# Optimization experiments

Measured on AMD Instinct MI355X. Metric: run time of the kernel, lower is better.

The kernel has to match this reference:

```python
import jax, jax.numpy as jnp
import numpy as np

B, S, H = 2, 2048, 2048
E, I, TOPK = 8, 1408, 2


def setup_inputs() -> dict:
    key = jax.random.key(0)
    k0, k1, k2, k3, k4 = jax.random.split(key, 5)
    return {
        "hidden_states": jax.random.normal(k0, (B, S, H), dtype=jnp.float32),
        "Wr": jax.random.normal(k1, (H, E), dtype=jnp.float32) * 0.02,
        "Wg": jax.random.normal(k2, (E, H, I), dtype=jnp.float32) * 0.02,
        "Wu": jax.random.normal(k3, (E, H, I), dtype=jnp.float32) * 0.02,
        "Wd": jax.random.normal(k4, (E, I, H), dtype=jnp.float32) * 0.02,
    }


def reference(hidden_states, Wr, Wg, Wu, Wd):
    b, s, h = hidden_states.shape
    x = hidden_states.reshape(-1, h)                      # [T, H]
    T = x.shape[0]
    router_logits = x @ Wr                                # [T, E]
    probs = jax.nn.softmax(router_logits.astype(jnp.float32), axis=-1)
    top_w, top_i = jax.lax.top_k(probs, TOPK)             # [T, k]
    top_w = top_w / jnp.sum(top_w, axis=-1, keepdims=True)  # norm_topk_prob
    top_w = top_w.astype(x.dtype)
    # combine weights per (token, expert): zero where expert not selected
    cw = jnp.zeros((T, E), dtype=x.dtype).at[
        jnp.arange(T)[:, None], top_i].add(top_w)         # [T, E]
    # per-expert SwiGLU MLP computed densely, masked/weighted by cw
    g = jax.nn.silu(jnp.einsum('th,ehi->tei', x, Wg))     # [T, E, I]
    u = jnp.einsum('th,ehi->tei', x, Wu)                  # [T, E, I]
    y = jnp.einsum('tei,eih->teh', g * u, Wd)             # [T, E, H]
    out = jnp.einsum('te,teh->th', cw, y)                 # [T, H]
    return out.reshape(b, s, h), router_logits
```

## Files before the change

### kernel.cpp

```cpp
#include <hip/hip_runtime.h>

#define T_TOK 4096
#define HD 2048
#define NE 8
#define NI 1408

typedef __bf16 bf16x8 __attribute__((ext_vector_type(8)));
typedef float f32x4 __attribute__((ext_vector_type(4)));
typedef unsigned short ushort8 __attribute__((ext_vector_type(8)));

#define S_WAITCNT_VMCNT(n) asm volatile("s_waitcnt vmcnt(" #n ")" ::: "memory")
__device__ __forceinline__ void wave_barrier() {
  asm volatile("" ::: "memory");
  __builtin_amdgcn_s_barrier();
  asm volatile("" ::: "memory");
}

__device__ __forceinline__ unsigned short f2bf(float f) {
  unsigned int u = __float_as_uint(f);
  u += 0x7FFFu + ((u >> 16) & 1u);
  return (unsigned short)(u >> 16);
}
__device__ __forceinline__ float bf2f(unsigned short u) {
  return __uint_as_float((unsigned int)u << 16);
}

__device__ __forceinline__ void gload_lds16(const void* g, void* l) {
  __builtin_amdgcn_global_load_lds(
      (const __attribute__((address_space(1))) unsigned int*)g,
      (__attribute__((address_space(3))) unsigned int*)l, 16, 0, 0);
}

__device__ __forceinline__ void transpose_body(const float* s,
                                               unsigned short* d,
                                               int R, int C, int r0, int c0) {
  int tid = threadIdx.x;
  int rg = tid & 7, cg = tid >> 3;
  const float* sb = s + (size_t)(r0 + rg * 8) * C + c0 + cg * 4;
  f32x4 v[8];
#pragma unroll
  for (int j = 0; j < 8; j++) v[j] = *(const f32x4*)(sb + (size_t)j * C);
  unsigned short* db = d + (size_t)(c0 + cg * 4) * R + r0 + rg * 8;
#pragma unroll
  for (int cc = 0; cc < 4; cc++) {
    ushort8 o;
#pragma unroll
    for (int j = 0; j < 8; j++) o[j] = f2bf(v[j][cc]);
    *(ushort8*)(db + (size_t)cc * R) = o;
  }
}

__global__ void prepass_kernel(const float* __restrict__ x,
                               const float* __restrict__ Wr,
                               const float* __restrict__ Wg,
                               const float* __restrict__ Wu,
                               const float* __restrict__ Wd,
                               float* __restrict__ logits,
                               unsigned short* __restrict__ xbf,
                               unsigned short* __restrict__ Wgt,
                               unsigned short* __restrict__ Wut,
                               unsigned short* __restrict__ Wdt,
                               int4* __restrict__ tokinfo,
                               int* __restrict__ cnt) {
  const int bid = blockIdx.x;
  if (bid < 1024) {
    int wv = threadIdx.x >> 6, lane = threadIdx.x & 63;
    int t = bid * 4 + wv;
    const float* xr = x + (size_t)t * HD;
    unsigned short* xbr = xbf + (size_t)t * HD;
    float acc[NE];
#pragma unroll
    for (int e = 0; e < NE; e++) acc[e] = 0.f;
    for (int hi = 0; hi < HD / 256; hi++) {
      int h = hi * 256 + lane * 4;
      f32x4 xv = *(const f32x4*)(xr + h);
      ushort4 o = { f2bf(xv[0]), f2bf(xv[1]), f2bf(xv[2]), f2bf(xv[3]) };
      *(ushort4*)(xbr + h) = o;
#pragma unroll
      for (int j = 0; j < 4; j++) {
        const float4* w4 = (const float4*)(Wr + (size_t)(h + j) * NE);
        float4 a = w4[0], b = w4[1];
        float xs = xv[j];
        acc[0] += xs * a.x; acc[1] += xs * a.y; acc[2] += xs * a.z; acc[3] += xs * a.w;
        acc[4] += xs * b.x; acc[5] += xs * b.y; acc[6] += xs * b.z; acc[7] += xs * b.w;
      }
    }
#pragma unroll
    for (int m = 32; m > 0; m >>= 1) {
#pragma unroll
      for (int e = 0; e < NE; e++) acc[e] += __shfl_xor(acc[e], m, 64);
    }
    if (lane < NE) logits[(size_t)t * NE + lane] = acc[lane];
    if (lane == 0) {
      int e0 = 0;
#pragma unroll
      for (int e = 1; e < NE; e++) if (acc[e] > acc[e0]) e0 = e;
      int e1 = (e0 == 0) ? 1 : 0;
#pragma unroll
      for (int e = 0; e < NE; e++) if (e != e0 && acc[e] > acc[e1]) e1 = e;
      float ex = expf(acc[e1] - acc[e0]);
      float w0 = 1.f / (1.f + ex);
      float w1 = ex / (1.f + ex);
      atomicAdd(&cnt[e0], 1);
      atomicAdd(&cnt[e1], 1);
      tokinfo[t] = make_int4(e0, e1, __float_as_int(w0), __float_as_int(w1));
    }
  } else if (bid < 1024 + 5632) {
    int r = bid - 1024;
    int xt = r % 11; r /= 11;
    int yt = r % 32; r /= 32;
    int e = r >> 1, sel = r & 1;
    const float* sp = (sel ? Wu : Wg) + (size_t)e * HD * NI;
    unsigned short* dp = (sel ? Wut : Wgt) + (size_t)e * HD * NI;
    transpose_body(sp, dp, HD, NI, yt * 64, xt * 128);
  } else {
    int r = bid - 1024 - 5632;
    int xt = r % 16; r /= 16;
    int yt = r % 22; r /= 22;
    int e = r;
    const float* sp = Wd + (size_t)e * NI * HD;
    unsigned short* dp = Wdt + (size_t)e * NI * HD;
    transpose_body(sp, dp, NI, HD, yt * 64, xt * 128);
  }
}

__global__ void route_finalize_kernel(const int4* __restrict__ tokinfo,
                                      int* __restrict__ cnt,
                                      int* __restrict__ row_tok,
                                      int2* __restrict__ tok2row) {
  if (threadIdx.x == 0) {
    int o = 0;
    for (int e = 0; e < NE; e++) { cnt[8 + e] = o; o += cnt[e]; }
  }
  __syncthreads();
  for (int t = threadIdx.x; t < T_TOK; t += 1024) {
    int4 info = tokinfo[t];
    int p0 = atomicAdd(&cnt[16 + info.x], 1);
    int r0 = cnt[8 + info.x] + p0;
    row_tok[r0] = t;
    int p1 = atomicAdd(&cnt[16 + info.y], 1);
    int r1 = cnt[8 + info.y] + p1;
    row_tok[r1] = t;
    tok2row[t] = make_int2(r0, r1);
  }
}

__launch_bounds__(256, 2)
__global__ void gemm1_kernel(const unsigned short* __restrict__ xbf,
                             const unsigned short* __restrict__ Wgt,
                             const unsigned short* __restrict__ Wut,
                             unsigned short* __restrict__ act,
                             const int* __restrict__ row_tok,
                             const int* __restrict__ cnt) {
  const int f = blockIdx.x + 11 * (blockIdx.y + 32 * blockIdx.z);
  const int e = f & 7;
  const int rem = f >> 3;
  const int nt = rem >> 5;
  const int mt = rem & 31;
  const int c = cnt[e];
  if (mt * 128 >= c) return;
  const int off = cnt[8 + e];
  const int rowbase = off + mt * 128, rowend = off + c;
  const int i0 = nt * 128;
  __shared__ __align__(16) char smem[73728];
  const int lane = threadIdx.x & 63, w = threadIdx.x >> 6;
  const int wr = w >> 1, wc = w & 1;

  const int rr0 = w * 16 + (lane >> 2);
  const int rr1 = rr0 + 64;
  const int q0 = (lane & 3) ^ ((rr0 >> 1) & 3);
  const int q1 = (lane & 3) ^ ((rr1 >> 1) & 3);
  int g0 = rowbase + rr0; if (g0 > rowend - 1) g0 = rowend - 1;
  int g1 = rowbase + rr1; if (g1 > rowend - 1) g1 = rowend - 1;
  const size_t tokA0 = (size_t)row_tok[g0] * HD;
  const size_t tokA1 = (size_t)row_tok[g1] * HD;
  const size_t bB0 = ((size_t)e * NI + i0 + rr0) * HD;
  const size_t bB1 = ((size_t)e * NI + i0 + rr1) * HD;
  const int ldsA = w * 1024;

  f32x4 zero = {0.f, 0.f, 0.f, 0.f};
  f32x4 accg[4][4], accu[4][4];
#pragma unroll
  for (int a = 0; a < 4; a++)
#pragma unroll
    for (int b = 0; b < 4; b++) { accg[a][b] = zero; accu[a][b] = zero; }

  auto stage = [&](int buf, int ks) {
    const int k0 = ks * 32;
    char* base = smem + buf * 24576;
    gload_lds16(xbf + tokA0 + k0 + q0 * 8, base + ldsA);
    gload_lds16(xbf + tokA1 + k0 + q1 * 8, base + ldsA + 4096);
    gload_lds16(Wgt + bB0 + k0 + q0 * 8, base + 8192 + ldsA);
    gload_lds16(Wgt + bB1 + k0 + q1 * 8, base + 8192 + ldsA + 4096);
    gload_lds16(Wut + bB0 + k0 + q0 * 8, base + 16384 + ldsA);
    gload_lds16(Wut + bB1 + k0 + q1 * 8, base + 16384 + ldsA + 4096);
  };
  const int rl = lane & 15, kslot = lane >> 4;
  auto compute = [&](int buf) {
    const char* base = smem + buf * 24576;
    bf16x8 af[4], bg[4], bu[4];
#pragma unroll
    for (int mi = 0; mi < 4; mi++) {
      int r = wr * 64 + mi * 16 + rl;
      int byt = r * 64 + ((kslot ^ ((r >> 1) & 3)) << 4);
      af[mi] = *(const bf16x8*)(base + byt);
    }
#pragma unroll
    for (int ni = 0; ni < 4; ni++) {
      int r = wc * 64 + ni * 16 + rl;
      int byt = r * 64 + ((kslot ^ ((r >> 1) & 3)) << 4);
      bg[ni] = *(const bf16x8*)(base + 8192 + byt);
      bu[ni] = *(const bf16x8*)(base + 16384 + byt);
    }
#pragma unroll
    for (int mi = 0; mi < 4; mi++)
#pragma unroll
      for (int ni = 0; ni < 4; ni++) {
        accg[mi][ni] = __builtin_amdgcn_mfma_f32_16x16x32_bf16(af[mi], bg[ni], accg[mi][ni], 0, 0, 0);
        accu[mi][ni] = __builtin_amdgcn_mfma_f32_16x16x32_bf16(af[mi], bu[ni], accu[mi][ni], 0, 0, 0);
      }
  };

  stage(0, 0);
  stage(1, 1);
  const int NKS = HD / 32;
  for (int ks = 0; ks < NKS; ks++) {
    if (ks < NKS - 1) {
      S_WAITCNT_VMCNT(6);
    } else {
      S_WAITCNT_VMCNT(0);
    }
    wave_barrier();
    if (ks + 2 < NKS) stage((ks + 2) % 3, ks + 2);
    compute(ks % 3);
  }

  const int rh = lane >> 4;
#pragma unroll
  for (int mi = 0; mi < 4; mi++)
#pragma unroll
    for (int ni = 0; ni < 4; ni++)
#pragma unroll
      for (int j = 0; j < 4; j++) {
        int grow = rowbase + wr * 64 + mi * 16 + rh * 4 + j;
        if (grow < rowend) {
          int gcol = i0 + wc * 64 + ni * 16 + rl;
          float g = accg[mi][ni][j], u = accu[mi][ni][j];
          float val = g / (1.f + __expf(-g)) * u;
          act[(size_t)grow * NI + gcol] = f2bf(val);
        }
      }
}

__launch_bounds__(256, 3)
__global__ void gemm2_kernel(const unsigned short* __restrict__ act,
                             const unsigned short* __restrict__ Wdt,
                             unsigned short* __restrict__ y,
                             const int* __restrict__ cnt) {
  const int f = blockIdx.x + 16 * (blockIdx.y + 32 * blockIdx.z);
  const int e = f & 7;
  const int rem = f >> 3;
  const int nt = rem >> 5;
  const int mt = rem & 31;
  const int c = cnt[e];
  if (mt * 128 >= c) return;
  const int off = cnt[8 + e];
  const int rowbase = off + mt * 128, rowend = off + c;
  const int n0 = nt * 128;
  __shared__ __align__(16) char smem[49152];
  const int lane = threadIdx.x & 63, w = threadIdx.x >> 6;
  const int wr = w >> 1, wc = w & 1;

  const int rr0 = w * 16 + (lane >> 2);
  const int rr1 = rr0 + 64;
  const int q0 = (lane & 3) ^ ((rr0 >> 1) & 3);
  const int q1 = (lane & 3) ^ ((rr1 >> 1) & 3);
  int g0 = rowbase + rr0; if (g0 > rowend - 1) g0 = rowend - 1;
  int g1 = rowbase + rr1; if (g1 > rowend - 1) g1 = rowend - 1;
  const size_t aA0 = (size_t)g0 * NI;
  const size_t aA1 = (size_t)g1 * NI;
  const size_t bB0 = ((size_t)e * HD + n0 + rr0) * NI;
  const size_t bB1 = ((size_t)e * HD + n0 + rr1) * NI;
  const int ldsA = w * 1024;

  f32x4 zero = {0.f, 0.f, 0.f, 0.f};
  f32x4 acc[4][4];
#pragma unroll
  for (int a = 0; a < 4; a++)
#pragma unroll
    for (int b = 0; b < 4; b++) acc[a][b] = zero;

  auto stage = [&](int buf, int ks) {
    const int k0 = ks * 32;
    char* base = smem + buf * 16384;
    gload_lds16(act + aA0 + k0 + q0 * 8, base + ldsA);
    gload_lds16(act + aA1 + k0 + q1 * 8, base + ldsA + 4096);
    gload_lds16(Wdt + bB0 + k0 + q0 * 8, base + 8192 + ldsA);
    gload_lds16(Wdt + bB1 + k0 + q1 * 8, base + 8192 + ldsA + 4096);
  };
  const int rl = lane & 15, kslot = lane >> 4;
  auto compute = [&](int buf) {
    const char* base = smem + buf * 16384;
    bf16x8 af[4], bf[4];
#pragma unroll
    for (int mi = 0; mi < 4; mi++) {
      int r = wr * 64 + mi * 16 + rl;
      int byt = r * 64 + ((kslot ^ ((r >> 1) & 3)) << 4);
      af[mi] = *(const bf16x8*)(base + byt);
    }
#pragma unroll
    for (int ni = 0; ni < 4; ni++) {
      int r = wc * 64 + ni * 16 + rl;
      int byt = r * 64 + ((kslot ^ ((r >> 1) & 3)) << 4);
      bf[ni] = *(const bf16x8*)(base + 8192 + byt);
    }
#pragma unroll
    for (int mi = 0; mi < 4; mi++)
#pragma unroll
      for (int ni = 0; ni < 4; ni++)
        acc[mi][ni] = __builtin_amdgcn_mfma_f32_16x16x32_bf16(af[mi], bf[ni], acc[mi][ni], 0, 0, 0);
  };

  stage(0, 0);
  stage(1, 1);
  const int NKS = NI / 32;
  for (int ks = 0; ks < NKS; ks++) {
    if (ks < NKS - 1) {
      S_WAITCNT_VMCNT(4);
    } else {
      S_WAITCNT_VMCNT(0);
    }
    wave_barrier();
    if (ks + 2 < NKS) stage((ks + 2) % 3, ks + 2);
    compute(ks % 3);
  }

  const int rh = lane >> 4;
#pragma unroll
  for (int mi = 0; mi < 4; mi++)
#pragma unroll
    for (int ni = 0; ni < 4; ni++)
#pragma unroll
      for (int j = 0; j < 4; j++) {
        int grow = rowbase + wr * 64 + mi * 16 + rh * 4 + j;
        if (grow < rowend) {
          int gcol = n0 + wc * 64 + ni * 16 + rl;
          y[(size_t)grow * HD + gcol] = f2bf(acc[mi][ni][j]);
        }
      }
}

__global__ void combine_kernel(const unsigned short* __restrict__ y,
                               const int2* __restrict__ tok2row,
                               const int4* __restrict__ tokinfo,
                               float* __restrict__ out) {
  int t = blockIdx.x, tid = threadIdx.x;
  int2 rr = tok2row[t];
  int4 info = tokinfo[t];
  float w0 = __int_as_float(info.z), w1 = __int_as_float(info.w);
  ushort8 a = ((const ushort8*)(y + (size_t)rr.x * HD))[tid];
  ushort8 b = ((const ushort8*)(y + (size_t)rr.y * HD))[tid];
  float4 o0, o1;
  o0.x = w0 * bf2f(a[0]) + w1 * bf2f(b[0]);
  o0.y = w0 * bf2f(a[1]) + w1 * bf2f(b[1]);
  o0.z = w0 * bf2f(a[2]) + w1 * bf2f(b[2]);
  o0.w = w0 * bf2f(a[3]) + w1 * bf2f(b[3]);
  o1.x = w0 * bf2f(a[4]) + w1 * bf2f(b[4]);
  o1.y = w0 * bf2f(a[5]) + w1 * bf2f(b[5]);
  o1.z = w0 * bf2f(a[6]) + w1 * bf2f(b[6]);
  o1.w = w0 * bf2f(a[7]) + w1 * bf2f(b[7]);
  float4* op = (float4*)(out + (size_t)t * HD + tid * 8);
  op[0] = o0; op[1] = o1;
}

extern "C" void kernel_launch(void* const* d_in, const int* in_sizes, int n_in,
                              void* d_out, int out_size, void* d_ws, size_t ws_size,
                              hipStream_t stream) {
  const float* x  = (const float*)d_in[0];
  const float* Wr = (const float*)d_in[1];
  const float* Wg = (const float*)d_in[2];
  const float* Wu = (const float*)d_in[3];
  const float* Wd = (const float*)d_in[4];
  float* out = (float*)d_out;
  char* ws = (char*)d_ws;

  unsigned short* xbf = (unsigned short*)(ws);
  unsigned short* Wgt = (unsigned short*)(ws + 16777216);
  unsigned short* Wut = (unsigned short*)(ws + 62914560);
  unsigned short* Wdt = (unsigned short*)(ws + 109051904);
  unsigned short* act = (unsigned short*)(ws + 155189248);
  unsigned short* yb  = (unsigned short*)(ws + 16777216);
  int4*  tokinfo      = (int4*)(ws + 178257920);
  int*   row_tok      = (int*)(ws + 178323456);
  int2*  tok2row      = (int2*)(ws + 178356224);
  int*   cnt          = (int*)(ws + 178388992);

  hipMemsetAsync(cnt, 0, 128, stream);

  prepass_kernel<<<1024 + 5632 + 2816, 256, 0, stream>>>(
      x, Wr, Wg, Wu, Wd, out + (size_t)T_TOK * HD, xbf, Wgt, Wut, Wdt,
      tokinfo, cnt);
  route_finalize_kernel<<<1, 1024, 0, stream>>>(tokinfo, cnt, row_tok, tok2row);

  gemm1_kernel<<<dim3(11, 32, NE), 256, 0, stream>>>(xbf, Wgt, Wut, act, row_tok, cnt);
  gemm2_kernel<<<dim3(16, 32, NE), 256, 0, stream>>>(act, Wdt, yb, cnt);
  combine_kernel<<<T_TOK, 256, 0, stream>>>(yb, tok2row, tokinfo, out);
}
```

Measured before the change: 459.2 us.

## Move Wd transpose into gemm1 grid to overlap with expert GEMM

Removes the Wd fp32→bf16 transpose from the prepass kernel and runs it instead as extra blocks appended to the gemm1 grid. The memory-bound transpose then overlaps with the compute-bound gate/up GEMM and fills slots left by early-exiting tiles. The cost is that gemm1 blocks now share CUs and bandwidth with transpose blocks. The prepass becomes shorter in exchange.

```diff
diff --git a/kernel.cpp b/kernel.cpp
--- a/kernel.cpp
+++ b/kernel.cpp
@@ -54,12 +54,10 @@
                                const float* __restrict__ Wr,
                                const float* __restrict__ Wg,
                                const float* __restrict__ Wu,
-                               const float* __restrict__ Wd,
                                float* __restrict__ logits,
                                unsigned short* __restrict__ xbf,
                                unsigned short* __restrict__ Wgt,
                                unsigned short* __restrict__ Wut,
-                               unsigned short* __restrict__ Wdt,
                                int4* __restrict__ tokinfo,
                                int* __restrict__ cnt) {
   const int bid = blockIdx.x;
@@ -105,7 +103,7 @@
       atomicAdd(&cnt[e1], 1);
       tokinfo[t] = make_int4(e0, e1, __float_as_int(w0), __float_as_int(w1));
     }
-  } else if (bid < 1024 + 5632) {
+  } else {
     int r = bid - 1024;
     int xt = r % 11; r /= 11;
     int yt = r % 32; r /= 32;
@@ -113,14 +111,6 @@
     const float* sp = (sel ? Wu : Wg) + (size_t)e * HD * NI;
     unsigned short* dp = (sel ? Wut : Wgt) + (size_t)e * HD * NI;
     transpose_body(sp, dp, HD, NI, yt * 64, xt * 128);
-  } else {
-    int r = bid - 1024 - 5632;
-    int xt = r % 16; r /= 16;
-    int yt = r % 22; r /= 22;
-    int e = r;
-    const float* sp = Wd + (size_t)e * NI * HD;
-    unsigned short* dp = Wdt + (size_t)e * NI * HD;
-    transpose_body(sp, dp, NI, HD, yt * 64, xt * 128);
   }
 }
 
@@ -149,14 +139,23 @@
 __global__ void gemm1_kernel(const unsigned short* __restrict__ xbf,
                              const unsigned short* __restrict__ Wgt,
                              const unsigned short* __restrict__ Wut,
+                             const float* __restrict__ Wd,
+                             unsigned short* __restrict__ Wdt,
                              unsigned short* __restrict__ act,
                              const int* __restrict__ row_tok,
                              const int* __restrict__ cnt) {
-  const int f = blockIdx.x + 11 * (blockIdx.y + 32 * blockIdx.z);
-  const int e = f & 7;
-  const int rem = f >> 3;
-  const int nt = rem >> 5;
-  const int mt = rem & 31;
+  const int F = blockIdx.x + 11 * (blockIdx.y + 32 * blockIdx.z);
+  const int e = F & 7;
+  const int r = F >> 3;
+  if (r >= 352) {
+    const int t = r - 352;
+    const int xt = t & 15, yt = t >> 4;
+    transpose_body(Wd + (size_t)e * NI * HD, Wdt + (size_t)e * NI * HD,
+                   NI, HD, yt * 64, xt * 128);
+    return;
+  }
+  const int nt = r >> 5;
+  const int mt = r & 31;
   const int c = cnt[e];
   if (mt * 128 >= c) return;
   const int off = cnt[8 + e];
@@ -201,14 +200,14 @@
     bf16x8 af[4], bg[4], bu[4];
 #pragma unroll
     for (int mi = 0; mi < 4; mi++) {
-      int r = wr * 64 + mi * 16 + rl;
-      int byt = r * 64 + ((kslot ^ ((r >> 1) & 3)) << 4);
+      int rr = wr * 64 + mi * 16 + rl;
+      int byt = rr * 64 + ((kslot ^ ((rr >> 1) & 3)) << 4);
       af[mi] = *(const bf16x8*)(base + byt);
     }
 #pragma unroll
     for (int ni = 0; ni < 4; ni++) {
-      int r = wc * 64 + ni * 16 + rl;
-      int byt = r * 64 + ((kslot ^ ((r >> 1) & 3)) << 4);
+      int rr = wc * 64 + ni * 16 + rl;
+      int byt = rr * 64 + ((kslot ^ ((rr >> 1) & 3)) << 4);
       bg[ni] = *(const bf16x8*)(base + 8192 + byt);
       bu[ni] = *(const bf16x8*)(base + 16384 + byt);
     }
@@ -304,14 +303,14 @@
     bf16x8 af[4], bf[4];
 #pragma unroll
     for (int mi = 0; mi < 4; mi++) {
-      int r = wr * 64 + mi * 16 + rl;
-      int byt = r * 64 + ((kslot ^ ((r >> 1) & 3)) << 4);
+      int rr = wr * 64 + mi * 16 + rl;
+      int byt = rr * 64 + ((kslot ^ ((rr >> 1) & 3)) << 4);
       af[mi] = *(const bf16x8*)(base + byt);
     }
 #pragma unroll
     for (int ni = 0; ni < 4; ni++) {
-      int r = wc * 64 + ni * 16 + rl;
-      int byt = r * 64 + ((kslot ^ ((r >> 1) & 3)) << 4);
+      int rr = wc * 64 + ni * 16 + rl;
+      int byt = rr * 64 + ((kslot ^ ((rr >> 1) & 3)) << 4);
       bf[ni] = *(const bf16x8*)(base + 8192 + byt);
     }
 #pragma unroll
@@ -397,12 +396,12 @@
 
   hipMemsetAsync(cnt, 0, 128, stream);
 
-  prepass_kernel<<<1024 + 5632 + 2816, 256, 0, stream>>>(
-      x, Wr, Wg, Wu, Wd, out + (size_t)T_TOK * HD, xbf, Wgt, Wut, Wdt,
-      tokinfo, cnt);
+  prepass_kernel<<<1024 + 5632, 256, 0, stream>>>(
+      x, Wr, Wg, Wu, out + (size_t)T_TOK * HD, xbf, Wgt, Wut, tokinfo, cnt);
   route_finalize_kernel<<<1, 1024, 0, stream>>>(tokinfo, cnt, row_tok, tok2row);
 
-  gemm1_kernel<<<dim3(11, 32, NE), 256, 0, stream>>>(xbf, Wgt, Wut, act, row_tok, cnt);
+  gemm1_kernel<<<dim3(11, 32, 16), 256, 0, stream>>>(
+      xbf, Wgt, Wut, Wd, Wdt, act, row_tok, cnt);
   gemm2_kernel<<<dim3(16, 32, NE), 256, 0, stream>>>(act, Wdt, yb, cnt);
   combine_kernel<<<T_TOK, 256, 0, stream>>>(yb, tok2row, tokinfo, out);
 }
```

After: 435.4 us. -5.2%, faster.
